# Kernel optimization log

Measured on AMD Instinct MI355X. Metric: run time of the kernel, lower is better.

Reference implementation:

```python
import jax, jax.numpy as jnp
import numpy as np

NUM_CODES = 4096
TEMPERATURE = 1.0
EPS = 1e-08


def setup_inputs() -> dict:
    key = jax.random.key(0)
    k1, k2, k3 = jax.random.split(key, 3)
    B, D, T = 16, 512, 1500
    encoder_stride = 320
    student_features = jax.random.normal(k1, (B, D, T), dtype=jnp.float32)
    codebook = jax.random.normal(k2, (NUM_CODES, D), dtype=jnp.float32)
    lengths = jax.random.randint(k3, (B,), 0, T * encoder_stride, dtype=jnp.int64)
    return {
        "student_features": student_features,
        "codebook": codebook,
        "lengths": lengths,
        "encoder_stride": encoder_stride,
    }


def _length_mask(lengths, T, stride):
    # frame t is valid iff t < floor(length / stride)  -> (B, T) float mask
    n_valid = jnp.minimum(lengths // stride, T)
    return (jnp.arange(T)[None, :] < n_valid[:, None]).astype(jnp.float32)


def reference(student_features, codebook, lengths, encoder_stride):
    B, D, T = student_features.shape
    mask = _length_mask(lengths, T, encoder_stride)            # (B, T)
    z = jnp.transpose(student_features, (0, 2, 1)).reshape(-1, D)  # (N, D), N = B*T
    # Euclidean cdist via ||z||^2 + ||c||^2 - 2 z c^T (same as torch.cdist GEMM path)
    z2 = jnp.sum(z * z, axis=-1, keepdims=True)                # (N, 1)
    c2 = jnp.sum(codebook * codebook, axis=-1)                 # (K,)
    d2 = z2 + c2[None, :] - 2.0 * (z @ codebook.T)             # (N, K)
    distances = jnp.sqrt(jnp.maximum(d2, 1e-12))
    logits = -distances / TEMPERATURE
    probs = jax.nn.softmax(logits, axis=-1)                    # (N, K)
    probs_masked = probs * mask.reshape(-1, 1)
    code_dist = jnp.sum(probs_masked, axis=0)                  # (K,)
    code_dist = code_dist / (jnp.sum(code_dist) + EPS)
    entropy = -jnp.sum(code_dist * jnp.log(code_dist + EPS))
    max_entropy = jnp.log(jnp.float32(NUM_CODES))
    return 1.0 - entropy / max_entropy
```

## Files before the change

### kernel.cpp

```cpp
#include <hip/hip_runtime.h>
#include <hip/hip_bf16.h>

#define NUM_B   16
#define DIM     512
#define TT      1500
#define NROWS   (NUM_B * TT)
#define NCODES  4096
#define ROW_TILES ((NROWS + 127) / 128)
#define NROWS_PAD (ROW_TILES * 128)
#define SHIFTC  30.0f

typedef __bf16 bf16x8 __attribute__((ext_vector_type(8)));
typedef float  floatx4 __attribute__((ext_vector_type(4)));
typedef unsigned short ushortx8 __attribute__((ext_vector_type(8)));

__device__ __forceinline__ void glds16(const void* g, void* l) {
    __builtin_amdgcn_global_load_lds(
        (__attribute__((address_space(1))) void*)(void*)g,
        (__attribute__((address_space(3))) void*)l, 16, 0, 0);
}

__global__ void k_transpose(const float* __restrict__ sf, unsigned short* __restrict__ zbf) {
    __shared__ float tile[32][33];
    int tid = threadIdx.x;
    int b = blockIdx.z, d0 = blockIdx.y * 32, t0 = blockIdx.x * 32;
    int tl = tid & 31, dg = tid >> 5;
#pragma unroll
    for (int p = 0; p < 4; ++p) {
        int dl = p * 8 + dg;
        int t = t0 + tl;
        if (t < TT) tile[tl][dl] = sf[(size_t)(b * DIM + d0 + dl) * TT + t];
    }
    __syncthreads();
    int dl = tid & 31, tg = tid >> 5;
#pragma unroll
    for (int p = 0; p < 4; ++p) {
        int tl2 = p * 8 + tg;
        int t = t0 + tl2;
        if (t < TT) {
            __hip_bfloat16 h = __float2bfloat16(tile[tl2][dl]);
            zbf[(size_t)(b * TT + t) * DIM + d0 + dl] = __builtin_bit_cast(unsigned short, h);
        }
    }
}

__global__ void k_z2(const unsigned short* __restrict__ zbf, float* __restrict__ z2) {
    int row = blockIdx.x * 4 + (threadIdx.x >> 6);
    int lane = threadIdx.x & 63;
    uint4 v = *(const uint4*)(zbf + (size_t)row * DIM + lane * 8);
    unsigned int u[4] = {v.x, v.y, v.z, v.w};
    float s = 0.f;
#pragma unroll
    for (int i = 0; i < 4; ++i) {
        float lo = __builtin_bit_cast(float, u[i] << 16);
        float hi = __builtin_bit_cast(float, u[i] & 0xffff0000u);
        s += lo * lo + hi * hi;
    }
#pragma unroll
    for (int off = 32; off >= 1; off >>= 1) s += __shfl_down(s, off);
    if (lane == 0) z2[row] = s;
}

__global__ void k_cb(const float* __restrict__ cb, unsigned short* __restrict__ cbbf,
                     float* __restrict__ c2) {
    int k = blockIdx.x * 4 + (threadIdx.x >> 6);
    int lane = threadIdx.x & 63;
    const float4* src = (const float4*)(cb + (size_t)k * DIM + lane * 8);
    float4 a = src[0], b2 = src[1];
    float vals[8] = {a.x, a.y, a.z, a.w, b2.x, b2.y, b2.z, b2.w};
    float s = 0.f;
    unsigned int h[8];
#pragma unroll
    for (int i = 0; i < 8; ++i) {
        __hip_bfloat16 hb = __float2bfloat16(vals[i]);
        h[i] = __builtin_bit_cast(unsigned short, hb);
        float vb = __bfloat162float(hb);
        s += vb * vb;
    }
    uint4 o;
    o.x = h[0] | (h[1] << 16); o.y = h[2] | (h[3] << 16);
    o.z = h[4] | (h[5] << 16); o.w = h[6] | (h[7] << 16);
    *(uint4*)(cbbf + (size_t)k * DIM + lane * 8) = o;
#pragma unroll
    for (int off = 32; off >= 1; off >>= 1) s += __shfl_down(s, off);
    if (lane == 0) c2[k] = s;
}

__global__ __launch_bounds__(256, 2) void k_gemm1(
    const unsigned short* __restrict__ zbf, const unsigned short* __restrict__ cbbf,
    const float* __restrict__ z2, const float* __restrict__ c2,
    const int* __restrict__ lengths, const int* __restrict__ stride_p,
    float* __restrict__ Sg, unsigned short* __restrict__ Eg) {
    __shared__ unsigned short As[128 * 64];
    __shared__ unsigned short Bs[128 * 64];
    __shared__ float z2s[128], c2s[128];
    __shared__ unsigned char vldp[128];
    __shared__ int s_any;
    int tid = threadIdx.x;
    int r0 = blockIdx.y * 128, c0 = blockIdx.x * 128;
    if (tid == 0) s_any = 0;
    __syncthreads();
    if (tid < 128) {
        int n = r0 + tid;
        int valid = 0;
        if (n < NROWS) {
            int b = n / TT, t = n - b * TT;
            int stride = stride_p[0];
            int nv = lengths[b] / stride;
            if (nv > TT) nv = TT;
            valid = (t < nv);
        }
        if (valid) atomicOr(&s_any, 1);
        vldp[tid] = (unsigned char)valid;
        z2s[tid] = z2[r0 + tid];
        c2s[tid] = c2[c0 + tid];
    }
    __syncthreads();
    if (!s_any) return;

    int wave = tid >> 6, lane = tid & 63;
    int l15 = lane & 15, l4 = lane >> 4;
    int wr = (wave >> 1) * 64, wc = (wave & 1) * 64;

    int srow = lane >> 3;
    int scg = (lane & 7) ^ srow;
    const unsigned short* ag = zbf + (size_t)(r0 + wave * 32 + srow) * DIM + scg * 8;
    const unsigned short* bg = cbbf + (size_t)(c0 + wave * 32 + srow) * DIM + scg * 8;
    unsigned short* al = As + (wave * 32) * 64;
    unsigned short* bl = Bs + (wave * 32) * 64;

    floatx4 acc[4][4];
    const floatx4 zero = {0.f, 0.f, 0.f, 0.f};
#pragma unroll
    for (int i = 0; i < 4; ++i)
#pragma unroll
        for (int j = 0; j < 4; ++j) acc[i][j] = zero;

    int sw = l15 & 7;

    for (int kc = 0; kc < 8; ++kc) {
#pragma unroll
        for (int q = 0; q < 4; ++q) {
            glds16(ag + (size_t)q * 8 * DIM + kc * 64, al + q * 8 * 64);
            glds16(bg + (size_t)q * 8 * DIM + kc * 64, bl + q * 8 * 64);
        }
        __syncthreads();
#pragma unroll
        for (int ks = 0; ks < 64; ks += 32) {
            int g = (ks >> 3) + l4;
            int pcg = g ^ sw;
            bf16x8 av[4], bv[4];
#pragma unroll
            for (int i = 0; i < 4; ++i)
                av[i] = __builtin_bit_cast(bf16x8,
                    *(const ushortx8*)&As[(wr + 16 * i + l15) * 64 + pcg * 8]);
#pragma unroll
            for (int j = 0; j < 4; ++j)
                bv[j] = __builtin_bit_cast(bf16x8,
                    *(const ushortx8*)&Bs[(wc + 16 * j + l15) * 64 + pcg * 8]);
#pragma unroll
            for (int i = 0; i < 4; ++i)
#pragma unroll
                for (int j = 0; j < 4; ++j)
                    acc[i][j] = __builtin_amdgcn_mfma_f32_16x16x32_bf16(av[i], bv[j], acc[i][j], 0, 0, 0);
        }
        __syncthreads();
    }

#pragma unroll
    for (int i = 0; i < 4; ++i) {
#pragma unroll
        for (int r = 0; r < 4; ++r) {
            int rl = wr + 16 * i + 4 * l4 + r;
            bool rv = vldp[rl] != 0;
            float z2v = z2s[rl];
            float s = 0.f;
            unsigned short* Ep = Eg + (size_t)(r0 + rl) * NCODES + c0 + wc + l15;
#pragma unroll
            for (int j = 0; j < 4; ++j) {
                int cl = wc + 16 * j + l15;
                float d2 = z2v + c2s[cl] - 2.0f * acc[i][j][r];
                float d = sqrtf(fmaxf(d2, 1e-12f));
                float e = __expf(SHIFTC - d);
                s += e;
                if (rv) Ep[16 * j] = __builtin_bit_cast(unsigned short, __float2bfloat16(e));
            }
            s += __shfl_xor(s, 1); s += __shfl_xor(s, 2);
            s += __shfl_xor(s, 4); s += __shfl_xor(s, 8);
            if (l15 == 0 && rv) atomicAdd(&Sg[r0 + rl], s);
        }
    }
}

__global__ __launch_bounds__(512) void k_scan(
    const unsigned short* __restrict__ Eg, const float* __restrict__ Sg,
    const int* __restrict__ lengths, const int* __restrict__ stride_p,
    float* __restrict__ cd) {
    __shared__ float rs[128];
    __shared__ int s_any;
    int tid = threadIdx.x;
    int r0 = blockIdx.y * 128;
    if (tid == 0) s_any = 0;
    __syncthreads();
    if (tid < 128) {
        int n = r0 + tid;
        int valid = 0;
        if (n < NROWS) {
            int b = n / TT, t = n - b * TT;
            int nv = lengths[b] / stride_p[0];
            if (nv > TT) nv = TT;
            valid = (t < nv);
        }
        if (valid) atomicOr(&s_any, 1);
        rs[tid] = valid ? 1.0f / Sg[n] : 0.0f;
    }
    __syncthreads();
    if (!s_any) return;

    int col0 = blockIdx.x * 2048 + (tid & 255) * 8;
    int rbase = (tid >> 8) * 64;
    float acc[8] = {0.f, 0.f, 0.f, 0.f, 0.f, 0.f, 0.f, 0.f};
    for (int nn = 0; nn < 64; ++nn) {
        float rn = rs[rbase + nn];
        if (rn == 0.f) continue;
        uint4 v = *(const uint4*)(Eg + (size_t)(r0 + rbase + nn) * NCODES + col0);
        unsigned int u[4] = {v.x, v.y, v.z, v.w};
#pragma unroll
        for (int q = 0; q < 4; ++q) {
            acc[2 * q]     += rn * __builtin_bit_cast(float, u[q] << 16);
            acc[2 * q + 1] += rn * __builtin_bit_cast(float, u[q] & 0xffff0000u);
        }
    }
#pragma unroll
    for (int t = 0; t < 8; ++t) atomicAdd(&cd[col0 + t], acc[t]);
}

template <int PASS>
__global__ __launch_bounds__(256, 2) void k_gemm(
    const unsigned short* __restrict__ zbf, const unsigned short* __restrict__ cbbf,
    const float* __restrict__ z2, const float* __restrict__ c2,
    const int* __restrict__ lengths, const int* __restrict__ stride_p,
    float* __restrict__ Sg, float* __restrict__ cd) {
    __shared__ unsigned short As[128 * 64];
    __shared__ unsigned short Bs[128 * 64];
    __shared__ float z2s[128], c2s[128], rs[128];
    __shared__ int s_any;
    int tid = threadIdx.x;
    int r0 = blockIdx.y * 128, c0 = blockIdx.x * 128;
    if (tid == 0) s_any = 0;
    __syncthreads();
    if (tid < 128) {
        int n = r0 + tid;
        int valid = 0;
        if (n < NROWS) {
            int b = n / TT, t = n - b * TT;
            int stride = stride_p[0];
            int nv = lengths[b] / stride;
            if (nv > TT) nv = TT;
            valid = (t < nv);
        }
        if (valid) atomicOr(&s_any, 1);
        z2s[tid] = z2[r0 + tid];
        c2s[tid] = c2[c0 + tid];
        if (PASS == 2) rs[tid] = valid ? (1.0f / Sg[r0 + tid]) : 0.0f;
    }
    __syncthreads();
    if (!s_any) return;

    int wave = tid >> 6, lane = tid & 63;
    int l15 = lane & 15, l4 = lane >> 4;
    int wr = (wave >> 1) * 64, wc = (wave & 1) * 64;
    int srow = lane >> 3;
    int scg = (lane & 7) ^ srow;
    const unsigned short* ag = zbf + (size_t)(r0 + wave * 32 + srow) * DIM + scg * 8;
    const unsigned short* bg = cbbf + (size_t)(c0 + wave * 32 + srow) * DIM + scg * 8;
    unsigned short* al = As + (wave * 32) * 64;
    unsigned short* bl = Bs + (wave * 32) * 64;

    floatx4 acc[4][4];
    const floatx4 zero = {0.f, 0.f, 0.f, 0.f};
#pragma unroll
    for (int i = 0; i < 4; ++i)
#pragma unroll
        for (int j = 0; j < 4; ++j) acc[i][j] = zero;
    int sw = l15 & 7;
    for (int kc = 0; kc < 8; ++kc) {
#pragma unroll
        for (int q = 0; q < 4; ++q) {
            glds16(ag + (size_t)q * 8 * DIM + kc * 64, al + q * 8 * 64);
            glds16(bg + (size_t)q * 8 * DIM + kc * 64, bl + q * 8 * 64);
        }
        __syncthreads();
#pragma unroll
        for (int ks = 0; ks < 64; ks += 32) {
            int g = (ks >> 3) + l4;
            int pcg = g ^ sw;
            bf16x8 av[4], bv[4];
#pragma unroll
            for (int i = 0; i < 4; ++i)
                av[i] = __builtin_bit_cast(bf16x8, *(const ushortx8*)&As[(wr + 16 * i + l15) * 64 + pcg * 8]);
#pragma unroll
            for (int j = 0; j < 4; ++j)
                bv[j] = __builtin_bit_cast(bf16x8, *(const ushortx8*)&Bs[(wc + 16 * j + l15) * 64 + pcg * 8]);
#pragma unroll
            for (int i = 0; i < 4; ++i)
#pragma unroll
                for (int j = 0; j < 4; ++j)
                    acc[i][j] = __builtin_amdgcn_mfma_f32_16x16x32_bf16(av[i], bv[j], acc[i][j], 0, 0, 0);
        }
        __syncthreads();
    }
    if (PASS == 1) {
#pragma unroll
        for (int i = 0; i < 4; ++i) {
#pragma unroll
            for (int r = 0; r < 4; ++r) {
                int rl = wr + 16 * i + 4 * l4 + r;
                float z2v = z2s[rl];
                float s = 0.f;
#pragma unroll
                for (int j = 0; j < 4; ++j) {
                    int cl = wc + 16 * j + l15;
                    float d2 = z2v + c2s[cl] - 2.0f * acc[i][j][r];
                    float d = sqrtf(fmaxf(d2, 1e-12f));
                    s += __expf(SHIFTC - d);
                }
                s += __shfl_xor(s, 1); s += __shfl_xor(s, 2);
                s += __shfl_xor(s, 4); s += __shfl_xor(s, 8);
                if (l15 == 0) atomicAdd(&Sg[r0 + rl], s);
            }
        }
    } else {
#pragma unroll
        for (int j = 0; j < 4; ++j) {
            int cl = wc + 16 * j + l15;
            float c2v = c2s[cl];
            float cs = 0.f;
#pragma unroll
            for (int i = 0; i < 4; ++i) {
#pragma unroll
                for (int r = 0; r < 4; ++r) {
                    int rl = wr + 16 * i + 4 * l4 + r;
                    float d2 = z2s[rl] + c2v - 2.0f * acc[i][j][r];
                    float d = sqrtf(fmaxf(d2, 1e-12f));
                    cs += __expf(SHIFTC - d) * rs[rl];
                }
            }
            cs += __shfl_xor(cs, 16); cs += __shfl_xor(cs, 32);
            if (l4 == 0) atomicAdd(&cd[c0 + cl], cs);
        }
    }
}

__global__ void k_final(const float* __restrict__ cd, float* __restrict__ out) {
    __shared__ float red[4];
    __shared__ float tot_s;
    int tid = threadIdx.x, lane = tid & 63, wave = tid >> 6;
    float t = 0.f;
    for (int i = tid; i < NCODES; i += 256) t += cd[i];
#pragma unroll
    for (int off = 32; off >= 1; off >>= 1) t += __shfl_down(t, off);
    if (lane == 0) red[wave] = t;
    __syncthreads();
    if (tid == 0) tot_s = red[0] + red[1] + red[2] + red[3];
    __syncthreads();
    float inv = 1.0f / (tot_s + 1e-8f);
    float e = 0.f;
    for (int i = tid; i < NCODES; i += 256) {
        float p = cd[i] * inv;
        e += p * __logf(p + 1e-8f);
    }
#pragma unroll
    for (int off = 32; off >= 1; off >>= 1) e += __shfl_down(e, off);
    if (lane == 0) red[wave] = e;
    __syncthreads();
    if (tid == 0) {
        float ent = -(red[0] + red[1] + red[2] + red[3]);
        out[0] = 1.0f - ent / __logf((float)NCODES);
    }
}

extern "C" void kernel_launch(void* const* d_in, const int* in_sizes, int n_in,
                              void* d_out, int out_size, void* d_ws, size_t ws_size,
                              hipStream_t stream) {
    const float* sf = (const float*)d_in[0];
    const float* cb = (const float*)d_in[1];
    const int* lengths = (const int*)d_in[2];
    const int* stride_p = (const int*)d_in[3];

    float* Sg = (float*)d_ws;
    float* cd = Sg + NROWS_PAD;
    float* z2 = cd + NCODES;
    float* c2 = z2 + NROWS_PAD;
    unsigned short* zbf = (unsigned short*)(c2 + NCODES);
    unsigned short* cbbf = zbf + (size_t)NROWS_PAD * DIM;
    unsigned short* Eg = cbbf + (size_t)NCODES * DIM;

    size_t base_bytes = (size_t)(2 * NROWS_PAD + 2 * NCODES) * 4
                      + ((size_t)NROWS_PAD * DIM + (size_t)NCODES * DIM) * 2;
    size_t need = base_bytes + (size_t)NROWS_PAD * NCODES * 2;

    hipMemsetAsync(Sg, 0, (size_t)(NROWS_PAD + NCODES) * sizeof(float), stream);
    k_transpose<<<dim3((TT + 31) / 32, DIM / 32, NUM_B), 256, 0, stream>>>(sf, zbf);
    k_cb<<<dim3(NCODES / 4), 256, 0, stream>>>(cb, cbbf, c2);
    k_z2<<<dim3(NROWS_PAD / 4), 256, 0, stream>>>(zbf, z2);
    if (ws_size >= need) {
        k_gemm1<<<dim3(NCODES / 128, ROW_TILES), 256, 0, stream>>>(zbf, cbbf, z2, c2, lengths, stride_p, Sg, Eg);
        k_scan<<<dim3(NCODES / 2048, ROW_TILES), 512, 0, stream>>>(Eg, Sg, lengths, stride_p, cd);
    } else {
        k_gemm<1><<<dim3(NCODES / 128, ROW_TILES), 256, 0, stream>>>(zbf, cbbf, z2, c2, lengths, stride_p, Sg, cd);
        k_gemm<2><<<dim3(NCODES / 128, ROW_TILES), 256, 0, stream>>>(zbf, cbbf, z2, c2, lengths, stride_p, Sg, cd);
    }
    k_final<<<1, 256, 0, stream>>>(cd, (float*)d_out);
}
```

Before: 251.5 us.

## Split scan reduction into slices, shrink scan rows per block, raise gemm occupancy

The scan kernel now handles 32 rows per block with 256 threads, giving many more blocks. Its column atomics are spread over 32 partial-sum slices of the code distribution, which the final kernel adds back together. This is meant to reduce atomic contention and improve parallelism in the reduction. The gemm kernels' launch bounds are raised to 4 blocks per CU, which may limit registers and cause spills. In gemm1, invalid rows are now skipped with an early continue rather than a predicated store.

```diff
diff --git a/kernel.cpp b/kernel.cpp
--- a/kernel.cpp
+++ b/kernel.cpp
@@ -8,6 +8,7 @@
 #define NCODES  4096
 #define ROW_TILES ((NROWS + 127) / 128)
 #define NROWS_PAD (ROW_TILES * 128)
+#define NSLICE  32
 #define SHIFTC  30.0f
 
 typedef __bf16 bf16x8 __attribute__((ext_vector_type(8)));
@@ -86,7 +87,7 @@
     if (lane == 0) c2[k] = s;
 }
 
-__global__ __launch_bounds__(256, 2) void k_gemm1(
+__global__ __launch_bounds__(256, 4) void k_gemm1(
     const unsigned short* __restrict__ zbf, const unsigned short* __restrict__ cbbf,
     const float* __restrict__ z2, const float* __restrict__ c2,
     const int* __restrict__ lengths, const int* __restrict__ stride_p,
@@ -172,7 +173,7 @@
 #pragma unroll
         for (int r = 0; r < 4; ++r) {
             int rl = wr + 16 * i + 4 * l4 + r;
-            bool rv = vldp[rl] != 0;
+            if (!vldp[rl]) continue;
             float z2v = z2s[rl];
             float s = 0.f;
             unsigned short* Ep = Eg + (size_t)(r0 + rl) * NCODES + c0 + wc + l15;
@@ -183,26 +184,26 @@
                 float d = sqrtf(fmaxf(d2, 1e-12f));
                 float e = __expf(SHIFTC - d);
                 s += e;
-                if (rv) Ep[16 * j] = __builtin_bit_cast(unsigned short, __float2bfloat16(e));
+                Ep[16 * j] = __builtin_bit_cast(unsigned short, __float2bfloat16(e));
             }
             s += __shfl_xor(s, 1); s += __shfl_xor(s, 2);
             s += __shfl_xor(s, 4); s += __shfl_xor(s, 8);
-            if (l15 == 0 && rv) atomicAdd(&Sg[r0 + rl], s);
-        }
-    }
-}
-
-__global__ __launch_bounds__(512) void k_scan(
+            if (l15 == 0) atomicAdd(&Sg[r0 + rl], s);
+        }
+    }
+}
+
+__global__ __launch_bounds__(256) void k_scan(
     const unsigned short* __restrict__ Eg, const float* __restrict__ Sg,
     const int* __restrict__ lengths, const int* __restrict__ stride_p,
-    float* __restrict__ cd) {
-    __shared__ float rs[128];
+    float* __restrict__ cdp) {
+    __shared__ float rs[32];
     __shared__ int s_any;
     int tid = threadIdx.x;
-    int r0 = blockIdx.y * 128;
+    int r0 = blockIdx.y * 32;
     if (tid == 0) s_any = 0;
     __syncthreads();
-    if (tid < 128) {
+    if (tid < 32) {
         int n = r0 + tid;
         int valid = 0;
         if (n < NROWS) {
@@ -217,13 +218,12 @@
     __syncthreads();
     if (!s_any) return;
 
-    int col0 = blockIdx.x * 2048 + (tid & 255) * 8;
-    int rbase = (tid >> 8) * 64;
+    int col0 = blockIdx.x * 2048 + tid * 8;
     float acc[8] = {0.f, 0.f, 0.f, 0.f, 0.f, 0.f, 0.f, 0.f};
-    for (int nn = 0; nn < 64; ++nn) {
-        float rn = rs[rbase + nn];
+    for (int nn = 0; nn < 32; ++nn) {
+        float rn = rs[nn];
         if (rn == 0.f) continue;
-        uint4 v = *(const uint4*)(Eg + (size_t)(r0 + rbase + nn) * NCODES + col0);
+        uint4 v = *(const uint4*)(Eg + (size_t)(r0 + nn) * NCODES + col0);
         unsigned int u[4] = {v.x, v.y, v.z, v.w};
 #pragma unroll
         for (int q = 0; q < 4; ++q) {
@@ -231,12 +231,13 @@
             acc[2 * q + 1] += rn * __builtin_bit_cast(float, u[q] & 0xffff0000u);
         }
     }
-#pragma unroll
-    for (int t = 0; t < 8; ++t) atomicAdd(&cd[col0 + t], acc[t]);
+    float* outp = cdp + (size_t)(blockIdx.y & (NSLICE - 1)) * NCODES;
+#pragma unroll
+    for (int t = 0; t < 8; ++t) atomicAdd(&outp[col0 + t], acc[t]);
 }
 
 template <int PASS>
-__global__ __launch_bounds__(256, 2) void k_gemm(
+__global__ __launch_bounds__(256, 4) void k_gemm(
     const unsigned short* __restrict__ zbf, const unsigned short* __restrict__ cbbf,
     const float* __restrict__ z2, const float* __restrict__ c2,
     const int* __restrict__ lengths, const int* __restrict__ stride_p,
@@ -352,12 +353,18 @@
     }
 }
 
-__global__ void k_final(const float* __restrict__ cd, float* __restrict__ out) {
+__global__ void k_final(float* __restrict__ cdp, float* __restrict__ out) {
     __shared__ float red[4];
     __shared__ float tot_s;
     int tid = threadIdx.x, lane = tid & 63, wave = tid >> 6;
     float t = 0.f;
-    for (int i = tid; i < NCODES; i += 256) t += cd[i];
+    for (int i = tid; i < NCODES; i += 256) {
+        float v = 0.f;
+#pragma unroll
+        for (int s = 0; s < NSLICE; ++s) v += cdp[(size_t)s * NCODES + i];
+        cdp[i] = v;
+        t += v;
+    }
 #pragma unroll
     for (int off = 32; off >= 1; off >>= 1) t += __shfl_down(t, off);
     if (lane == 0) red[wave] = t;
@@ -367,7 +374,7 @@
     float inv = 1.0f / (tot_s + 1e-8f);
     float e = 0.f;
     for (int i = tid; i < NCODES; i += 256) {
-        float p = cd[i] * inv;
+        float p = cdp[i] * inv;
         e += p * __logf(p + 1e-8f);
     }
 #pragma unroll
@@ -389,27 +396,28 @@
     const int* stride_p = (const int*)d_in[3];
 
     float* Sg = (float*)d_ws;
-    float* cd = Sg + NROWS_PAD;
-    float* z2 = cd + NCODES;
+    float* cdp = Sg + NROWS_PAD;
+    float* z2 = cdp + (size_t)NSLICE * NCODES;
     float* c2 = z2 + NROWS_PAD;
     unsigned short* zbf = (unsigned short*)(c2 + NCODES);
     unsigned short* cbbf = zbf + (size_t)NROWS_PAD * DIM;
     unsigned short* Eg = cbbf + (size_t)NCODES * DIM;
 
-    size_t base_bytes = (size_t)(2 * NROWS_PAD + 2 * NCODES) * 4
+    size_t base_bytes = (size_t)(2 * NROWS_PAD + NCODES) * 4
+                      + (size_t)NSLICE * NCODES * 4
                       + ((size_t)NROWS_PAD * DIM + (size_t)NCODES * DIM) * 2;
     size_t need = base_bytes + (size_t)NROWS_PAD * NCODES * 2;
 
-    hipMemsetAsync(Sg, 0, (size_t)(NROWS_PAD + NCODES) * sizeof(float), stream);
+    hipMemsetAsync(Sg, 0, ((size_t)NROWS_PAD + (size_t)NSLICE * NCODES) * sizeof(float), stream);
     k_transpose<<<dim3((TT + 31) / 32, DIM / 32, NUM_B), 256, 0, stream>>>(sf, zbf);
     k_cb<<<dim3(NCODES / 4), 256, 0, stream>>>(cb, cbbf, c2);
     k_z2<<<dim3(NROWS_PAD / 4), 256, 0, stream>>>(zbf, z2);
     if (ws_size >= need) {
         k_gemm1<<<dim3(NCODES / 128, ROW_TILES), 256, 0, stream>>>(zbf, cbbf, z2, c2, lengths, stride_p, Sg, Eg);
-        k_scan<<<dim3(NCODES / 2048, ROW_TILES), 512, 0, stream>>>(Eg, Sg, lengths, stride_p, cd);
+        k_scan<<<dim3(NCODES / 2048, NROWS_PAD / 32), 256, 0, stream>>>(Eg, Sg, lengths, stride_p, cdp);
     } else {
-        k_gemm<1><<<dim3(NCODES / 128, ROW_TILES), 256, 0, stream>>>(zbf, cbbf, z2, c2, lengths, stride_p, Sg, cd);
-        k_gemm<2><<<dim3(NCODES / 128, ROW_TILES), 256, 0, stream>>>(zbf, cbbf, z2, c2, lengths, stride_p, Sg, cd);
-    }
-    k_final<<<1, 256, 0, stream>>>(cd, (float*)d_out);
-}
+        k_gemm<1><<<dim3(NCODES / 128, ROW_TILES), 256, 0, stream>>>(zbf, cbbf, z2, c2, lengths, stride_p, Sg, cdp);
+        k_gemm<2><<<dim3(NCODES / 128, ROW_TILES), 256, 0, stream>>>(zbf, cbbf, z2, c2, lengths, stride_p, Sg, cdp);
+    }
+    k_final<<<1, 256, 0, stream>>>(cdp, (float*)d_out);
+}
```

Result: slower. 263.1 us (+4.6%).
